# Performance work log

Hardware: AMD Instinct MI355X
Metric: run time of the kernel (lower is better)

Reference implementation:

```python
import jax, jax.numpy as jnp
import numpy as np

# Hardware-emulation constants (from init_kwargs, NeuroSim-style QLinear)
WL_IN = 8        # input activation bit width (bit-serial)
WL_W = 8         # weight bit width
CELL_BIT = 2     # bits per memory cell -> 4 weight slices
SUB = 128        # crossbar sub-array size (rows summed in analog)
ADC_BITS = 5     # ADC precision per partial sum
ONOFF = 10.0     # cell on/off conductance ratio
VARI = 0.05      # multiplicative device variation sigma


def _adc_quant(x, bits, axes):
    # LinearQuantizeOut: uniform quantization between tensor min/max
    mn = jnp.min(x, axis=axes, keepdims=True)
    mx = jnp.max(x, axis=axes, keepdims=True)
    step = (mx - mn) * (2.0 ** (-bits))
    step = jnp.where(step <= 0, 1.0, step)
    idx = jnp.clip(jnp.floor((x - mn) / step), 0.0, 2.0 ** bits - 1.0)
    return idx * step + mn


def _qlinear_hw(x, w, noise):
    """Analog PIM crossbar emulation of y = x @ w.T with bit-serial inputs,
    bit-sliced cells, on/off-ratio offset + dummy column, device variation,
    per-subarray ADC quantization."""
    B, N = x.shape
    F = w.shape[0]
    I, W, K = WL_IN, WL_W, WL_W // CELL_BIT
    cr = 2.0 ** CELL_BIT
    lower, upper = 1.0 / ONOFF, 1.0
    S = (N + SUB - 1) // SUB
    Np = S * SUB
    # quantize input to I bits in [0,1]; weight to W-bit integer in [0, 2^W-1]
    xq = jnp.round(jnp.clip(x, 0.0, 1.0) * (2.0 ** I - 1.0))            # [B, N]
    Xi = jnp.clip(jnp.round((w + 1.0) * 0.5 * (2.0 ** W - 1.0)), 0.0, 2.0 ** W - 1.0)  # [F, N]
    xq = jnp.pad(xq, ((0, 0), (0, Np - N)))
    Xi = jnp.pad(Xi, ((0, 0), (0, Np - N)))
    zpow = 2.0 ** jnp.arange(I, dtype=x.dtype)
    kpow = cr ** jnp.arange(K, dtype=x.dtype)
    bits = jnp.mod(jnp.floor(xq[..., None] / zpow), 2.0)                # [B, Np, I]
    slc = jnp.mod(jnp.floor(Xi[..., None] / kpow), cr)                  # [F, Np, K]
    g = slc * (upper - lower) + (cr - 1.0) * lower                      # cell conductances
    g = g * (1.0 + VARI * noise)                                        # device variation
    bits = bits.reshape(B, S, SUB, I)
    g = g.reshape(F, S, SUB, K)
    # analog partial sums per (input bit i, subarray s, weight slice k)
    P = jnp.einsum('bsai,fsak->iskbf', bits, g)                         # [I,S,K,B,F]
    # dummy column (all cells at lowest conductance), identical across F
    D = jnp.transpose(bits.sum(axis=2), (2, 1, 0)) * ((cr - 1.0) * lower)  # [I,S,B]
    Pq = _adc_quant(P, ADC_BITS, axes=(3, 4))
    Dq = _adc_quant(D, ADC_BITS, axes=(2,))
    scal = (2.0 ** jnp.arange(I, dtype=x.dtype))[:, None] * (cr ** jnp.arange(K, dtype=x.dtype))[None, :]
    acc = jnp.einsum('iskbf,ik->bf', Pq - Dq[:, :, None, :, None], scal) / (upper - lower)
    # undo integer mappings: w = 2*Xi/(2^W-1) - 1, x = xq/(2^I-1)
    out = 2.0 * acc / ((2.0 ** I - 1.0) * (2.0 ** W - 1.0)) \
          - xq.sum(axis=1, keepdims=True) / (2.0 ** I - 1.0)
    return out


def _qlinear(x, w, noise):
    # straight-through quantized weight (WAGE-style STE) + hardware forward
    Xi = jnp.clip(jnp.round((w + 1.0) * 0.5 * (2.0 ** WL_W - 1.0)), 0.0, 2.0 ** WL_W - 1.0)
    wq = 2.0 * Xi / (2.0 ** WL_W - 1.0) - 1.0
    wq_ste = w + jax.lax.stop_gradient(wq - w)
    out_ideal = x @ wq_ste.T
    out_hw = _qlinear_hw(x, w, noise)
    return out_ideal + jax.lax.stop_gradient(out_hw - out_ideal)


def setup_inputs() -> dict:
    key = jax.random.key(0)
    k1, k2, k3, k4, k5 = jax.random.split(key, 5)
    x = jax.random.uniform(k1, (1024, 784), dtype=jnp.float32)
    w1 = jax.random.normal(k2, (512, 784), dtype=jnp.float32) * 0.05
    w3 = jax.random.normal(k3, (10, 512), dtype=jnp.float32) * 0.08
    noise1 = jax.random.normal(k4, (512, 896, 4), dtype=jnp.float32)  # 784 padded to 7*128
    noise3 = jax.random.normal(k5, (10, 512, 4), dtype=jnp.float32)   # 512 = 4*128 exact
    return {"x": x, "w1": w1, "w3": w3, "noise1": noise1, "noise3": noise3}


def reference(x, w1, w3, noise1, noise3):
    h = jnp.tanh(_qlinear(x, w1, noise1))   # QLinear(784,512) + Tanh
    return _qlinear(h, w3, noise3)          # QLinear(512,10)
```

## Files before the change

kernel.cpp:

```cpp
#include <hip/hip_runtime.h>

#define FLTMAX 3.402823466e+38f


__global__ void prep1_kernel(const float* __restrict__ x, float* __restrict__ sx1,
                             unsigned* __restrict__ xqbT, unsigned* __restrict__ stats1)
{
    __shared__ float xr[896];
    __shared__ float red[128];
    int b = blockIdx.x;
    if (b == 0) {
        for (int t = threadIdx.x; t < 224; t += 128) {
            stats1[t * 2] = 0x7F7FFFFFu; stats1[t * 2 + 1] = 0u;
        }
    }
    float psum = 0.f;
    for (int n = threadIdx.x; n < 896; n += 128) {
        float v = 0.f;
        if (n < 784) {
            float xv = x[b * 784 + n];
            xv = fminf(fmaxf(xv, 0.f), 1.f);
            v = rintf(__fmul_rn(xv, 255.f));
        }
        xr[n] = v;
        psum += v;
    }
    red[threadIdx.x] = psum;
    __syncthreads();
    for (int w = 64; w >= 1; w >>= 1) {
        if (threadIdx.x < w) red[threadIdx.x] += red[threadIdx.x + w];
        __syncthreads();
    }
    if (threadIdx.x == 0) sx1[b] = red[0];
    if (threadIdx.x < 28) {
        int w = threadIdx.x;
        unsigned words[8] = {0, 0, 0, 0, 0, 0, 0, 0};
#pragma unroll 8
        for (int n = 0; n < 32; ++n) {
            int v = (int)xr[w * 32 + n];
#pragma unroll
            for (int i = 0; i < 8; ++i) words[i] |= ((unsigned)((v >> i) & 1)) << n;
        }
#pragma unroll
        for (int i = 0; i < 8; ++i) xqbT[(i * 28 + w) * 1024 + b] = words[i];
    }
}

__global__ void prepg1t_kernel(const float* __restrict__ w1, const float* __restrict__ noise1,
                               float* __restrict__ g1t)
{
    __shared__ float t[4][32][33];
    const int n0 = blockIdx.x * 32, f0 = blockIdx.y * 32;
    const int tid = threadIdx.x;
    {
        int n = tid & 31, fi = tid >> 5;
#pragma unroll
        for (int p = 0; p < 4; ++p) {
            int f = p * 8 + fi;
            int gn = n0 + n, gf = f0 + f;
            float gv[4] = {0.f, 0.f, 0.f, 0.f};
            if (gn < 784) {
                float w = w1[gf * 784 + gn];
                float Xi = fminf(fmaxf(rintf(__fmul_rn(__fmul_rn(__fadd_rn(w, 1.f), 0.5f), 255.f)),
                                       0.f), 255.f);
                int xi = (int)Xi;
                float4 nz = *(const float4*)&noise1[(gf * 896 + gn) * 4];
                float nzv[4] = {nz.x, nz.y, nz.z, nz.w};
#pragma unroll
                for (int k = 0; k < 4; ++k) {
                    int slc = (xi >> (2 * k)) & 3;
                    float base = __fadd_rn(__fmul_rn((float)slc, 0.9f), 0.3f);
                    float nf = __fadd_rn(1.f, __fmul_rn(0.05f, nzv[k]));
                    gv[k] = __fmul_rn(base, nf);
                }
            }
#pragma unroll
            for (int k = 0; k < 4; ++k) t[k][n][f] = gv[k];
        }
    }
    __syncthreads();
    {
        int f = tid & 31, nn = tid >> 5;
#pragma unroll
        for (int p = 0; p < 4; ++p) {
            int n = p * 8 + nn;
#pragma unroll
            for (int k = 0; k < 4; ++k)
                g1t[(n0 + n) * 2048 + k * 512 + f0 + f] = t[k][n][f];
        }
    }
}

__global__ void prepg2_kernel(const float* __restrict__ w3, const float* __restrict__ noise3,
                              float* __restrict__ g2t)
{
    int gid = blockIdx.x * 256 + threadIdx.x;
    if (gid >= 10 * 512) return;
    int f = gid / 512, n = gid % 512;
    float w = w3[f * 512 + n];
    float Xi = fminf(fmaxf(rintf(__fmul_rn(__fmul_rn(__fadd_rn(w, 1.f), 0.5f), 255.f)),
                           0.f), 255.f);
    int xi = (int)Xi;
#pragma unroll
    for (int k = 0; k < 4; ++k) {
        int slc = (xi >> (2 * k)) & 3;
        float base = __fadd_rn(__fmul_rn((float)slc, 0.9f), 0.3f);
        float nf = __fadd_rn(1.f, __fmul_rn(0.05f, noise3[(f * 512 + n) * 4 + k]));
        g2t[n * 40 + k * 10 + f] = __fmul_rn(base, nf);
    }
}

__global__ void dqpopT_kernel(const unsigned* __restrict__ xqbT, float* __restrict__ Dq)
{
    __shared__ float red[512];
    const int i = blockIdx.x / 7, s = blockIdx.x % 7;
    const int tid = threadIdx.x;
    float D[4];
    float mn = FLTMAX, mx = -FLTMAX;
#pragma unroll
    for (int u = 0; u < 4; ++u) {
        int b = tid + u * 256;
        int c = 0;
#pragma unroll
        for (int w = 0; w < 4; ++w)
            c += __popc(xqbT[(i * 28 + s * 4 + w) * 1024 + b]);
        D[u] = __fmul_rn((float)c, 0.3f);
        mn = fminf(mn, D[u]);
        mx = fmaxf(mx, D[u]);
    }
    red[tid] = mn; red[256 + tid] = mx;
    __syncthreads();
    for (int w = 128; w >= 1; w >>= 1) {
        if (tid < w) {
            red[tid] = fminf(red[tid], red[tid + w]);
            red[256 + tid] = fmaxf(red[256 + tid], red[256 + tid + w]);
        }
        __syncthreads();
    }
    mn = red[0]; mx = red[256];
    float step = __fmul_rn(__fsub_rn(mx, mn), 0.03125f);
    if (step <= 0.f) step = 1.f;
#pragma unroll
    for (int u = 0; u < 4; ++u) {
        int b = tid + u * 256;
        float idx = fminf(fmaxf(floorf(__fdiv_rn(__fsub_rn(D[u], mn), step)), 0.f), 31.f);
        Dq[(i * 7 + s) * 1024 + b] = __fadd_rn(__fmul_rn(idx, step), mn);
    }
}

__global__ void dqpop_kernel(const unsigned* __restrict__ xqb, float* __restrict__ Dq,
                             int S, int wpr)
{
    __shared__ float red[512];
    const int i = blockIdx.x / S, s = blockIdx.x % S;
    const int tid = threadIdx.x;
    float D[4];
    float mn = FLTMAX, mx = -FLTMAX;
#pragma unroll
    for (int u = 0; u < 4; ++u) {
        int b = tid + u * 256;
        uint4 w = *(const uint4*)&xqb[(i * 1024 + b) * wpr + s * 4];
        int c = __popc(w.x) + __popc(w.y) + __popc(w.z) + __popc(w.w);
        D[u] = __fmul_rn((float)c, 0.3f);
        mn = fminf(mn, D[u]);
        mx = fmaxf(mx, D[u]);
    }
    red[tid] = mn; red[256 + tid] = mx;
    __syncthreads();
    for (int w = 128; w >= 1; w >>= 1) {
        if (tid < w) {
            red[tid] = fminf(red[tid], red[tid + w]);
            red[256 + tid] = fmaxf(red[256 + tid], red[256 + tid + w]);
        }
        __syncthreads();
    }
    mn = red[0]; mx = red[256];
    float step = __fmul_rn(__fsub_rn(mx, mn), 0.03125f);
    if (step <= 0.f) step = 1.f;
#pragma unroll
    for (int u = 0; u < 4; ++u) {
        int b = tid + u * 256;
        float idx = fminf(fmaxf(floorf(__fdiv_rn(__fsub_rn(D[u], mn), step)), 0.f), 31.f);
        Dq[(i * S + s) * 1024 + b] = __fadd_rn(__fmul_rn(idx, step), mn);
    }
}

#define BK 32
__global__ __launch_bounds__(256, 4) void mm1_kernel(
    const unsigned* __restrict__ xqbT, const float* __restrict__ g1t,
    float* __restrict__ P, unsigned* __restrict__ stats, int s0)
{
    __shared__ __align__(16) float Bs[BK][132];
    __shared__ unsigned Abits[128];
    __shared__ float red[512];
    const int tid = threadIdx.x;
    const int sl = blockIdx.x >> 6;
    const int r = blockIdx.x & 63;
    const int i = r >> 3;
    const int b0 = (r & 7) * 128;
    const int s = s0 + sl;
    const int colBase = blockIdx.y * 128;
    const int tx = tid & 15, ty = tid >> 4;

    const int aB = tid >> 5;
    const int eB = (tid & 31) << 2;

    float4 pB[4];
    unsigned pAw = 0;
#pragma unroll
    for (int u = 0; u < 4; ++u)
        pB[u] = *(const float4*)&g1t[(s * 128 + u * 8 + aB) * 2048 + colBase + eB];
    if (tid < 128) pAw = xqbT[(i * 28 + s * 4) * 1024 + b0 + tid];

    float acc[8][8] = {};

    for (int ac = 0; ac < 4; ++ac) {
        __syncthreads();
#pragma unroll
        for (int u = 0; u < 4; ++u)
            *(float4*)&Bs[u * 8 + aB][eB] = pB[u];
        if (tid < 128) Abits[tid] = pAw;
        __syncthreads();

        if (ac < 3) {
            const int n0 = s * 128 + (ac + 1) * BK;
#pragma unroll
            for (int u = 0; u < 4; ++u)
                pB[u] = *(const float4*)&g1t[(n0 + u * 8 + aB) * 2048 + colBase + eB];
            if (tid < 128) pAw = xqbT[(i * 28 + s * 4 + ac + 1) * 1024 + b0 + tid];
        }

        unsigned wrd[8];
#pragma unroll
        for (int u = 0; u < 4; ++u) {
            wrd[u]     = Abits[(ty << 2) + u];
            wrd[4 + u] = Abits[64 + (ty << 2) + u];
        }

#pragma unroll 4
        for (int a = 0; a < BK; ++a) {
            float br[8];
            *(float4*)&br[0] = *(const float4*)&Bs[a][(tx << 2)];
            *(float4*)&br[4] = *(const float4*)&Bs[a][64 + (tx << 2)];
#pragma unroll
            for (int u = 0; u < 8; ++u) {
                float ab = (float)((wrd[u] >> a) & 1u);
#pragma unroll
                for (int v = 0; v < 8; ++v)
                    acc[u][v] = fmaf(ab, br[v], acc[u][v]);
            }
        }
    }

#pragma unroll
    for (int uh = 0; uh < 2; ++uh)
#pragma unroll
        for (int u = 0; u < 4; ++u) {
            int row = (sl * 8 + i) * 1024 + b0 + uh * 64 + (ty << 2) + u;
#pragma unroll
            for (int vh = 0; vh < 2; ++vh) {
                float4 v = make_float4(acc[uh * 4 + u][vh * 4 + 0], acc[uh * 4 + u][vh * 4 + 1],
                                       acc[uh * 4 + u][vh * 4 + 2], acc[uh * 4 + u][vh * 4 + 3]);
                *(float4*)&P[(size_t)row * 2048 + colBase + vh * 64 + (tx << 2)] = v;
            }
        }

    float mn = acc[0][0], mx = acc[0][0];
#pragma unroll
    for (int u = 0; u < 8; ++u)
#pragma unroll
        for (int v = 0; v < 8; ++v) { mn = fminf(mn, acc[u][v]); mx = fmaxf(mx, acc[u][v]); }
    red[tid] = mn; red[256 + tid] = mx;
    __syncthreads();
    for (int w = 128; w >= 1; w >>= 1) {
        if (tid < w) {
            red[tid] = fminf(red[tid], red[tid + w]);
            red[256 + tid] = fmaxf(red[256 + tid], red[256 + tid + w]);
        }
        __syncthreads();
    }
    if (tid == 0) {
        int k = colBase >> 9;
        int slot = ((s * 8 + i) * 4 + k) * 2;
        atomicMin(&stats[slot], __float_as_uint(red[0]));
        atomicMax(&stats[slot + 1], __float_as_uint(red[256]));
    }
}

__global__ void quantpack_kernel(const float* __restrict__ P,
                                 const unsigned* __restrict__ stats,
                                 unsigned char* __restrict__ Pidx, int s0)
{
    __shared__ unsigned stage[1024];
    const int t = blockIdx.x;
    const int q = t & 3;
    const int btile = (t >> 2) & 7;
    const int colgrp = (t >> 5) & 15;
    const int pi = t >> 9;
    const int sl = pi >> 3, i = pi & 7;
    const int s = s0 + sl;
    const int k = colgrp >> 2;
    const int slot = ((s * 8 + i) * 4 + k) * 2;
    const float mn = __uint_as_float(stats[slot]);
    const float mx = __uint_as_float(stats[slot + 1]);
    float step = __fmul_rn(__fsub_rn(mx, mn), 0.03125f);
    if (step <= 0.f) step = 1.f;

    const int tid = threadIdx.x;
    const int rsub = tid >> 5;
    const int c0 = (tid & 31) << 2;
#pragma unroll
    for (int j = 0; j < 4; ++j) {
        int row = q * 32 + j * 8 + rsub;
        float4 v = *(const float4*)&P[((size_t)(pi * 1024 + btile * 128 + row)) * 2048
                                      + colgrp * 128 + c0];
        float ix;
        unsigned pack;
        ix = fminf(fmaxf(floorf(__fdiv_rn(__fsub_rn(v.x, mn), step)), 0.f), 31.f);
        pack = (unsigned)(int)ix;
        ix = fminf(fmaxf(floorf(__fdiv_rn(__fsub_rn(v.y, mn), step)), 0.f), 31.f);
        pack |= (unsigned)(int)ix << 8;
        ix = fminf(fmaxf(floorf(__fdiv_rn(__fsub_rn(v.z, mn), step)), 0.f), 31.f);
        pack |= (unsigned)(int)ix << 16;
        ix = fminf(fmaxf(floorf(__fdiv_rn(__fsub_rn(v.w, mn), step)), 0.f), 31.f);
        pack |= (unsigned)(int)ix << 24;
        stage[j * 256 + tid] = pack;
    }
    __syncthreads();
    unsigned char* tbase = Pidx +
        ((size_t)(((s * 8 + i) * 16 + colgrp) * 8 + btile)) * 16384 + q * 4096;
    const unsigned* sp = &stage[tid * 4];
    *(uint4*)&tbase[tid * 16] = make_uint4(sp[0], sp[1], sp[2], sp[3]);
}

__global__ void fold1_kernel(const unsigned char* __restrict__ Pidx,
                             const unsigned* __restrict__ stats,
                             const float* __restrict__ Dq1, const float* __restrict__ sx1,
                             float* __restrict__ xq2, unsigned* __restrict__ xqb2,
                             float* __restrict__ sx2)
{
    __shared__ float red[512];
    __shared__ float dt;
    __shared__ float2 st[224];
    int b = blockIdx.x;
    int f = threadIdx.x;
    if (f < 224) {
        float mn = __uint_as_float(stats[f * 2]);
        float mx = __uint_as_float(stats[f * 2 + 1]);
        float step = __fmul_rn(__fsub_rn(mx, mn), 0.03125f);
        if (step <= 0.f) step = 1.f;
        st[f] = make_float2(mn, step);
    }
    if (f == 0) {
        float sd = 0.f;
        for (int i = 0; i < 8; ++i) {
            float sc = (float)(85 << i);
            for (int ss = 0; ss < 7; ++ss) sd = fmaf(Dq1[(i * 7 + ss) * 1024 + b], sc, sd);
        }
        dt = sd;
    }
    __syncthreads();
    const int fhi = f >> 7, fl = f & 127;
    const unsigned char* pb = Pidx + (size_t)(b >> 7) * 16384
                                   + (size_t)(b & 127) * 128 + fl;
    float accR = 0.f;
    for (int s = 0; s < 7; ++s) {
        float sum = 0.f;
        for (int i = 0; i < 8; ++i) {
            const int si16 = (s * 8 + i) * 16;
#pragma unroll
            for (int kk = 0; kk < 4; ++kk) {
                float2 ms = st[((s * 8 + i) << 2) + kk];
                float ixv = (float)pb[(size_t)(si16 + kk * 4 + fhi) * 131072];
                float pq = __fadd_rn(__fmul_rn(ixv, ms.y), ms.x);
                sum = fmaf(pq, (float)(1 << (i + 2 * kk)), sum);
            }
        }
        accR = __fadd_rn(accR, sum);
    }
    float total = __fsub_rn(accR, dt);
    float acc = __fdiv_rn(total, 0.9f);
    float o = __fsub_rn(__fdiv_rn(__fmul_rn(2.f, acc), 65025.f), __fdiv_rn(sx1[b], 255.f));
    float h = tanhf(o);
    h = fminf(fmaxf(h, 0.f), 1.f);
    float code = rintf(__fmul_rn(h, 255.f));
    xq2[b * 512 + f] = code;
    int ci = (int)code;
    int lane = f & 63;
#pragma unroll
    for (int i = 0; i < 8; ++i) {
        unsigned long long m = __ballot((ci >> i) & 1);
        if ((lane & 31) == 0) {
            unsigned wv = (lane & 32) ? (unsigned)(m >> 32) : (unsigned)m;
            xqb2[(i * 1024 + b) * 16 + (f >> 5)] = wv;
        }
    }
    red[f] = code;
    __syncthreads();
    for (int w = 256; w >= 1; w >>= 1) {
        if (f < w) red[f] += red[f + w];
        __syncthreads();
    }
    if (f == 0) sx2[b] = red[0];
}

__global__ void mm2_kernel(const float* __restrict__ xq2, const float* __restrict__ g2t,
                           float* __restrict__ P2)
{
    int gid = blockIdx.x * 256 + threadIdx.x;
    if (gid >= 40960) return;
    int f = gid % 10;
    int b = (gid / 10) & 1023;
    int s = gid / 10240;
    float acc[8][4] = {};
    for (int a = 0; a < 128; ++a) {
        int n = s * 128 + a;
        int xi = (int)xq2[b * 512 + n];
        float g0 = g2t[n * 40 + f];
        float gA = g2t[n * 40 + 10 + f];
        float gB = g2t[n * 40 + 20 + f];
        float gC = g2t[n * 40 + 30 + f];
#pragma unroll
        for (int i = 0; i < 8; ++i) {
            float bi = (float)((xi >> i) & 1);
            acc[i][0] = fmaf(bi, g0, acc[i][0]);
            acc[i][1] = fmaf(bi, gA, acc[i][1]);
            acc[i][2] = fmaf(bi, gB, acc[i][2]);
            acc[i][3] = fmaf(bi, gC, acc[i][3]);
        }
    }
#pragma unroll
    for (int i = 0; i < 8; ++i)
#pragma unroll
        for (int k = 0; k < 4; ++k)
            P2[(size_t)((s * 8 + i) * 4 + k) * 10240 + b * 10 + f] = acc[i][k];
}

__global__ void stat2_kernel(const float* __restrict__ P2, float2* __restrict__ stats2)
{
    __shared__ float red[512];
    int p = blockIdx.x;
    int tid = threadIdx.x;
    float mn = FLTMAX, mx = -FLTMAX;
    for (int t = tid; t < 10240; t += 256) {
        float v = P2[(size_t)p * 10240 + t];
        mn = fminf(mn, v); mx = fmaxf(mx, v);
    }
    red[tid] = mn; red[256 + tid] = mx;
    __syncthreads();
    for (int w = 128; w >= 1; w >>= 1) {
        if (tid < w) {
            red[tid] = fminf(red[tid], red[tid + w]);
            red[256 + tid] = fmaxf(red[256 + tid], red[256 + tid + w]);
        }
        __syncthreads();
    }
    if (tid == 0) {
        float step = __fmul_rn(__fsub_rn(red[256], red[0]), 0.03125f);
        if (step <= 0.f) step = 1.f;
        stats2[p] = make_float2(red[0], step);
    }
}

__global__ void out2_kernel(const float* __restrict__ P2, const float2* __restrict__ stats2,
                            const float* __restrict__ Dq2, const float* __restrict__ sx2,
                            float* __restrict__ out)
{
    int gid = blockIdx.x * 256 + threadIdx.x;
    if (gid >= 10240) return;
    int b = gid / 10;
    float dt = 0.f;
    for (int i = 0; i < 8; ++i) {
        float sc = (float)(85 << i);
        for (int s = 0; s < 4; ++s) dt = fmaf(Dq2[(i * 4 + s) * 1024 + b], sc, dt);
    }
    float sum = 0.f;
    for (int s = 0; s < 4; ++s)
        for (int i = 0; i < 8; ++i)
#pragma unroll
            for (int k = 0; k < 4; ++k) {
                int p = (s * 8 + i) * 4 + k;
                float2 st = stats2[p];
                float val = P2[(size_t)p * 10240 + gid];
                float idx = fminf(fmaxf(floorf(__fdiv_rn(__fsub_rn(val, st.x), st.y)), 0.f), 31.f);
                float pq = __fadd_rn(__fmul_rn(idx, st.y), st.x);
                sum = fmaf(pq, (float)(1 << (i + 2 * k)), sum);
            }
    float total = __fsub_rn(sum, dt);
    float acc = __fdiv_rn(total, 0.9f);
    out[gid] = __fsub_rn(__fdiv_rn(__fmul_rn(2.f, acc), 65025.f), __fdiv_rn(sx2[b], 255.f));
}

extern "C" void kernel_launch(void* const* d_in, const int* in_sizes, int n_in,
                              void* d_out, int out_size, void* d_ws, size_t ws_size,
                              hipStream_t stream)
{
    const float* x      = (const float*)d_in[0];
    const float* w1     = (const float*)d_in[1];
    const float* w3     = (const float*)d_in[2];
    const float* noise1 = (const float*)d_in[3];
    const float* noise3 = (const float*)d_in[4];
    float* out = (float*)d_out;
    float* ws  = (float*)d_ws;

    float*         g1t    = ws + 0;
    float*         xq2    = ws + 1835008;
    float*         P2     = ws + 2359296;
    float*         g2t    = ws + 3670016;
    float*         Dq1    = ws + 3690496;
    float*         Dq2    = ws + 3747840;
    float*         sx1    = ws + 3780608;
    float*         sx2    = ws + 3781632;
    float2*        stats2 = (float2*)(ws + 3782656);
    unsigned*      stats1 = (unsigned*)(ws + 3782912);
    unsigned*      xqbT   = (unsigned*)(ws + 3783424);
    unsigned*      xqb2   = (unsigned*)(ws + 4012800);
    unsigned char* Pidx   = (unsigned char*)(ws + 4143872);
    float*         Ps     = ws + 33504000;

    const size_t fixedf = 33504000;
    const size_t planef = 16777216;
    int G = 1;
    while (G < 7 && (fixedf + (size_t)(G + 1) * planef) * sizeof(float) <= ws_size) ++G;

    prep1_kernel<<<1024, 128, 0, stream>>>(x, sx1, xqbT, stats1);
    prepg1t_kernel<<<dim3(28, 16), 256, 0, stream>>>(w1, noise1, g1t);
    dqpopT_kernel<<<56, 256, 0, stream>>>(xqbT, Dq1);

    for (int s0 = 0; s0 < 7;) {
        int Gc = (7 - s0 < G) ? (7 - s0) : G;
        mm1_kernel<<<dim3(Gc * 64, 16), 256, 0, stream>>>(xqbT, g1t, Ps, stats1, s0);
        quantpack_kernel<<<Gc * 4096, 256, 0, stream>>>(Ps, stats1, Pidx, s0);
        s0 += Gc;
    }

    fold1_kernel<<<1024, 512, 0, stream>>>(Pidx, stats1, Dq1, sx1, xq2, xqb2, sx2);
    prepg2_kernel<<<20, 256, 0, stream>>>(w3, noise3, g2t);
    dqpop_kernel<<<32, 256, 0, stream>>>(xqb2, Dq2, 4, 16);
    mm2_kernel<<<160, 256, 0, stream>>>(xq2, g2t, P2);
    stat2_kernel<<<128, 256, 0, stream>>>(P2, stats2);
    out2_kernel<<<40, 256, 0, stream>>>(P2, stats2, Dq2, sx2, out);
}
```

Baseline: 691.4 us.

## Software-pipeline mm1 and quantpack across subarrays in one fused launch

Merges the mm1 matmul and the quantize/pack step into one kernel whose grid holds both kinds of block. Each launch computes the partial-sum plane of subarray s and quantizes the plane of subarray s-1, ping-ponging between two buffers, with a final launch for the last plane. The aim is to overlap the compute-bound matmul with the memory-bound quantization and to keep each plane small enough to stay in cache. The cost is fixed 8 launches instead of possibly 2, and a fixed two-plane workspace footprint that replaces the earlier grouping sized from the available workspace.

```diff
diff --git a/kernel.cpp b/kernel.cpp
--- a/kernel.cpp
+++ b/kernel.cpp
@@ -186,151 +186,147 @@
 }
 
 #define BK 32
-__global__ __launch_bounds__(256, 4) void mm1_kernel(
+__global__ __launch_bounds__(256, 4) void mm1q_kernel(
     const unsigned* __restrict__ xqbT, const float* __restrict__ g1t,
-    float* __restrict__ P, unsigned* __restrict__ stats, int s0)
+    float* __restrict__ Pcur, const float* __restrict__ Pprev,
+    unsigned* __restrict__ stats, unsigned char* __restrict__ Pidx,
+    int s, int ps)
 {
     __shared__ __align__(16) float Bs[BK][132];
     __shared__ unsigned Abits[128];
     __shared__ float red[512];
+    __shared__ unsigned stage[1024];
     const int tid = threadIdx.x;
-    const int sl = blockIdx.x >> 6;
-    const int r = blockIdx.x & 63;
-    const int i = r >> 3;
-    const int b0 = (r & 7) * 128;
-    const int s = s0 + sl;
-    const int colBase = blockIdx.y * 128;
-    const int tx = tid & 15, ty = tid >> 4;
-
-    const int aB = tid >> 5;
-    const int eB = (tid & 31) << 2;
-
-    float4 pB[4];
-    unsigned pAw = 0;
-#pragma unroll
-    for (int u = 0; u < 4; ++u)
-        pB[u] = *(const float4*)&g1t[(s * 128 + u * 8 + aB) * 2048 + colBase + eB];
-    if (tid < 128) pAw = xqbT[(i * 28 + s * 4) * 1024 + b0 + tid];
-
-    float acc[8][8] = {};
-
-    for (int ac = 0; ac < 4; ++ac) {
-        __syncthreads();
+    const int nmm = (s >= 0) ? 1024 : 0;
+
+    if ((int)blockIdx.x < nmm) {
+        const int bid = blockIdx.x;
+        const int r = bid & 63;
+        const int i = r >> 3;
+        const int b0 = (r & 7) * 128;
+        const int colBase = (bid >> 6) * 128;
+        const int tx = tid & 15, ty = tid >> 4;
+        const int aB = tid >> 5;
+        const int eB = (tid & 31) << 2;
+
+        float4 pB[4];
+        unsigned pAw = 0;
 #pragma unroll
         for (int u = 0; u < 4; ++u)
-            *(float4*)&Bs[u * 8 + aB][eB] = pB[u];
-        if (tid < 128) Abits[tid] = pAw;
-        __syncthreads();
-
-        if (ac < 3) {
-            const int n0 = s * 128 + (ac + 1) * BK;
+            pB[u] = *(const float4*)&g1t[(s * 128 + u * 8 + aB) * 2048 + colBase + eB];
+        if (tid < 128) pAw = xqbT[(i * 28 + s * 4) * 1024 + b0 + tid];
+
+        float acc[8][8] = {};
+
+        for (int ac = 0; ac < 4; ++ac) {
+            __syncthreads();
 #pragma unroll
             for (int u = 0; u < 4; ++u)
-                pB[u] = *(const float4*)&g1t[(n0 + u * 8 + aB) * 2048 + colBase + eB];
-            if (tid < 128) pAw = xqbT[(i * 28 + s * 4 + ac + 1) * 1024 + b0 + tid];
-        }
-
-        unsigned wrd[8];
-#pragma unroll
-        for (int u = 0; u < 4; ++u) {
-            wrd[u]     = Abits[(ty << 2) + u];
-            wrd[4 + u] = Abits[64 + (ty << 2) + u];
-        }
+                *(float4*)&Bs[u * 8 + aB][eB] = pB[u];
+            if (tid < 128) Abits[tid] = pAw;
+            __syncthreads();
+
+            if (ac < 3) {
+                const int n0 = s * 128 + (ac + 1) * BK;
+#pragma unroll
+                for (int u = 0; u < 4; ++u)
+                    pB[u] = *(const float4*)&g1t[(n0 + u * 8 + aB) * 2048 + colBase + eB];
+                if (tid < 128) pAw = xqbT[(i * 28 + s * 4 + ac + 1) * 1024 + b0 + tid];
+            }
+
+            unsigned wrd[8];
+#pragma unroll
+            for (int u = 0; u < 4; ++u) {
+                wrd[u]     = Abits[(ty << 2) + u];
+                wrd[4 + u] = Abits[64 + (ty << 2) + u];
+            }
 
 #pragma unroll 4
-        for (int a = 0; a < BK; ++a) {
-            float br[8];
-            *(float4*)&br[0] = *(const float4*)&Bs[a][(tx << 2)];
-            *(float4*)&br[4] = *(const float4*)&Bs[a][64 + (tx << 2)];
-#pragma unroll
-            for (int u = 0; u < 8; ++u) {
-                float ab = (float)((wrd[u] >> a) & 1u);
-#pragma unroll
-                for (int v = 0; v < 8; ++v)
-                    acc[u][v] = fmaf(ab, br[v], acc[u][v]);
-            }
-        }
-    }
-
-#pragma unroll
-    for (int uh = 0; uh < 2; ++uh)
-#pragma unroll
-        for (int u = 0; u < 4; ++u) {
-            int row = (sl * 8 + i) * 1024 + b0 + uh * 64 + (ty << 2) + u;
-#pragma unroll
-            for (int vh = 0; vh < 2; ++vh) {
-                float4 v = make_float4(acc[uh * 4 + u][vh * 4 + 0], acc[uh * 4 + u][vh * 4 + 1],
-                                       acc[uh * 4 + u][vh * 4 + 2], acc[uh * 4 + u][vh * 4 + 3]);
-                *(float4*)&P[(size_t)row * 2048 + colBase + vh * 64 + (tx << 2)] = v;
-            }
-        }
-
-    float mn = acc[0][0], mx = acc[0][0];
-#pragma unroll
-    for (int u = 0; u < 8; ++u)
-#pragma unroll
-        for (int v = 0; v < 8; ++v) { mn = fminf(mn, acc[u][v]); mx = fmaxf(mx, acc[u][v]); }
-    red[tid] = mn; red[256 + tid] = mx;
-    __syncthreads();
-    for (int w = 128; w >= 1; w >>= 1) {
-        if (tid < w) {
-            red[tid] = fminf(red[tid], red[tid + w]);
-            red[256 + tid] = fmaxf(red[256 + tid], red[256 + tid + w]);
-        }
-        __syncthreads();
-    }
-    if (tid == 0) {
-        int k = colBase >> 9;
-        int slot = ((s * 8 + i) * 4 + k) * 2;
-        atomicMin(&stats[slot], __float_as_uint(red[0]));
-        atomicMax(&stats[slot + 1], __float_as_uint(red[256]));
-    }
-}
-
-__global__ void quantpack_kernel(const float* __restrict__ P,
-                                 const unsigned* __restrict__ stats,
-                                 unsigned char* __restrict__ Pidx, int s0)
-{
-    __shared__ unsigned stage[1024];
-    const int t = blockIdx.x;
-    const int q = t & 3;
-    const int btile = (t >> 2) & 7;
-    const int colgrp = (t >> 5) & 15;
-    const int pi = t >> 9;
-    const int sl = pi >> 3, i = pi & 7;
-    const int s = s0 + sl;
-    const int k = colgrp >> 2;
-    const int slot = ((s * 8 + i) * 4 + k) * 2;
-    const float mn = __uint_as_float(stats[slot]);
-    const float mx = __uint_as_float(stats[slot + 1]);
-    float step = __fmul_rn(__fsub_rn(mx, mn), 0.03125f);
-    if (step <= 0.f) step = 1.f;
-
-    const int tid = threadIdx.x;
-    const int rsub = tid >> 5;
-    const int c0 = (tid & 31) << 2;
-#pragma unroll
-    for (int j = 0; j < 4; ++j) {
-        int row = q * 32 + j * 8 + rsub;
-        float4 v = *(const float4*)&P[((size_t)(pi * 1024 + btile * 128 + row)) * 2048
-                                      + colgrp * 128 + c0];
-        float ix;
-        unsigned pack;
-        ix = fminf(fmaxf(floorf(__fdiv_rn(__fsub_rn(v.x, mn), step)), 0.f), 31.f);
-        pack = (unsigned)(int)ix;
-        ix = fminf(fmaxf(floorf(__fdiv_rn(__fsub_rn(v.y, mn), step)), 0.f), 31.f);
-        pack |= (unsigned)(int)ix << 8;
-        ix = fminf(fmaxf(floorf(__fdiv_rn(__fsub_rn(v.z, mn), step)), 0.f), 31.f);
-        pack |= (unsigned)(int)ix << 16;
-        ix = fminf(fmaxf(floorf(__fdiv_rn(__fsub_rn(v.w, mn), step)), 0.f), 31.f);
-        pack |= (unsigned)(int)ix << 24;
-        stage[j * 256 + tid] = pack;
-    }
-    __syncthreads();
-    unsigned char* tbase = Pidx +
-        ((size_t)(((s * 8 + i) * 16 + colgrp) * 8 + btile)) * 16384 + q * 4096;
-    const unsigned* sp = &stage[tid * 4];
-    *(uint4*)&tbase[tid * 16] = make_uint4(sp[0], sp[1], sp[2], sp[3]);
+            for (int a = 0; a < BK; ++a) {
+                float br[8];
+                *(float4*)&br[0] = *(const float4*)&Bs[a][(tx << 2)];
+                *(float4*)&br[4] = *(const float4*)&Bs[a][64 + (tx << 2)];
+#pragma unroll
+                for (int u = 0; u < 8; ++u) {
+                    float ab = (float)((wrd[u] >> a) & 1u);
+#pragma unroll
+                    for (int v = 0; v < 8; ++v)
+                        acc[u][v] = fmaf(ab, br[v], acc[u][v]);
+                }
+            }
+        }
+
+#pragma unroll
+        for (int uh = 0; uh < 2; ++uh)
+#pragma unroll
+            for (int u = 0; u < 4; ++u) {
+                int row = i * 1024 + b0 + uh * 64 + (ty << 2) + u;
+#pragma unroll
+                for (int vh = 0; vh < 2; ++vh) {
+                    float4 v = make_float4(acc[uh * 4 + u][vh * 4 + 0], acc[uh * 4 + u][vh * 4 + 1],
+                                           acc[uh * 4 + u][vh * 4 + 2], acc[uh * 4 + u][vh * 4 + 3]);
+                    *(float4*)&Pcur[(size_t)row * 2048 + colBase + vh * 64 + (tx << 2)] = v;
+                }
+            }
+
+        float mn = acc[0][0], mx = acc[0][0];
+#pragma unroll
+        for (int u = 0; u < 8; ++u)
+#pragma unroll
+            for (int v = 0; v < 8; ++v) { mn = fminf(mn, acc[u][v]); mx = fmaxf(mx, acc[u][v]); }
+        red[tid] = mn; red[256 + tid] = mx;
+        __syncthreads();
+        for (int w = 128; w >= 1; w >>= 1) {
+            if (tid < w) {
+                red[tid] = fminf(red[tid], red[tid + w]);
+                red[256 + tid] = fmaxf(red[256 + tid], red[256 + tid + w]);
+            }
+            __syncthreads();
+        }
+        if (tid == 0) {
+            int k = colBase >> 9;
+            int slot = ((s * 8 + i) * 4 + k) * 2;
+            atomicMin(&stats[slot], __float_as_uint(red[0]));
+            atomicMax(&stats[slot + 1], __float_as_uint(red[256]));
+        }
+    } else if (ps >= 0) {
+        const int t = blockIdx.x - nmm;
+        const int q = t & 3;
+        const int btile = (t >> 2) & 7;
+        const int colgrp = (t >> 5) & 15;
+        const int i = t >> 9;
+        const int k = colgrp >> 2;
+        const int slot = ((ps * 8 + i) * 4 + k) * 2;
+        const float mn = __uint_as_float(stats[slot]);
+        const float mx = __uint_as_float(stats[slot + 1]);
+        float step = __fmul_rn(__fsub_rn(mx, mn), 0.03125f);
+        if (step <= 0.f) step = 1.f;
+
+        const int rsub = tid >> 5;
+        const int c0 = (tid & 31) << 2;
+#pragma unroll
+        for (int j = 0; j < 4; ++j) {
+            int row = q * 32 + j * 8 + rsub;
+            float4 v = *(const float4*)&Pprev[((size_t)(i * 1024 + btile * 128 + row)) * 2048
+                                              + colgrp * 128 + c0];
+            float ix;
+            unsigned pack;
+            ix = fminf(fmaxf(floorf(__fdiv_rn(__fsub_rn(v.x, mn), step)), 0.f), 31.f);
+            pack = (unsigned)(int)ix;
+            ix = fminf(fmaxf(floorf(__fdiv_rn(__fsub_rn(v.y, mn), step)), 0.f), 31.f);
+            pack |= (unsigned)(int)ix << 8;
+            ix = fminf(fmaxf(floorf(__fdiv_rn(__fsub_rn(v.z, mn), step)), 0.f), 31.f);
+            pack |= (unsigned)(int)ix << 16;
+            ix = fminf(fmaxf(floorf(__fdiv_rn(__fsub_rn(v.w, mn), step)), 0.f), 31.f);
+            pack |= (unsigned)(int)ix << 24;
+            stage[j * 256 + tid] = pack;
+        }
+        __syncthreads();
+        unsigned char* tbase = Pidx +
+            ((size_t)(((ps * 8 + i) * 16 + colgrp) * 8 + btile)) * 16384 + q * 4096;
+        const unsigned* sp = &stage[tid * 4];
+        *(uint4*)&tbase[tid * 16] = make_uint4(sp[0], sp[1], sp[2], sp[3]);
+    }
 }
 
 __global__ void fold1_kernel(const unsigned char* __restrict__ Pidx,
@@ -516,23 +512,21 @@
     unsigned*      xqbT   = (unsigned*)(ws + 3783424);
     unsigned*      xqb2   = (unsigned*)(ws + 4012800);
     unsigned char* Pidx   = (unsigned char*)(ws + 4143872);
-    float*         Ps     = ws + 33504000;
-
-    const size_t fixedf = 33504000;
-    const size_t planef = 16777216;
-    int G = 1;
-    while (G < 7 && (fixedf + (size_t)(G + 1) * planef) * sizeof(float) <= ws_size) ++G;
+    float*         PsA    = ws + 33504000;
+    float*         PsB    = ws + 50281216;
 
     prep1_kernel<<<1024, 128, 0, stream>>>(x, sx1, xqbT, stats1);
     prepg1t_kernel<<<dim3(28, 16), 256, 0, stream>>>(w1, noise1, g1t);
     dqpopT_kernel<<<56, 256, 0, stream>>>(xqbT, Dq1);
 
-    for (int s0 = 0; s0 < 7;) {
-        int Gc = (7 - s0 < G) ? (7 - s0) : G;
-        mm1_kernel<<<dim3(Gc * 64, 16), 256, 0, stream>>>(xqbT, g1t, Ps, stats1, s0);
-        quantpack_kernel<<<Gc * 4096, 256, 0, stream>>>(Ps, stats1, Pidx, s0);
-        s0 += Gc;
-    }
+    float* buf[2] = { PsA, PsB };
+    for (int s = 0; s < 7; ++s) {
+        int nqp = (s > 0) ? 4096 : 0;
+        mm1q_kernel<<<1024 + nqp, 256, 0, stream>>>(
+            xqbT, g1t, buf[s & 1], buf[(s ^ 1) & 1], stats1, Pidx, s, s - 1);
+    }
+    mm1q_kernel<<<4096, 256, 0, stream>>>(
+        xqbT, g1t, nullptr, buf[0] , stats1, Pidx, -1, 6);
 
     fold1_kernel<<<1024, 512, 0, stream>>>(Pidx, stats1, Dq1, sx1, xq2, xqb2, sx2);
     prepg2_kernel<<<20, 256, 0, stream>>>(w3, noise3, g2t);
```

Measured after the change: 722.8 us. 1.05x slower.
